# Performance work log

Measured on AMD Instinct MI355X. Metric: run time of the kernel, lower is better.

## Reference

```python
import jax, jax.numpy as jnp
import numpy as np

B, A, F, D, C = 256, 128, 512, 6, 512  # batch, max_atoms, atom_features, max_degree, conv_width


def setup_inputs() -> dict:
    key = jax.random.key(0)
    k1, k2, k3, k4 = jax.random.split(key, 4)
    atoms = jax.random.normal(k1, (B, A, F), dtype=jnp.float32)
    # neighbour indices in [0, A); pad entries beyond each atom's degree with -1
    neigh = jax.random.randint(k2, (B, A, D), 0, A)
    deg = jax.random.randint(k3, (B, A, 1), 0, D)  # degrees in 0..D-1
    bonds = jnp.where(jnp.arange(D)[None, None, :] < deg, neigh, -1)
    # one Dense(conv_width) per degree: stacked kernels [D, F, C] and biases [D, C]
    W = jax.random.normal(k4, (D, F, C), dtype=jnp.float32) * 0.02
    b = jnp.zeros((D, C), dtype=jnp.float32)
    return {"atoms": atoms, "bonds": bonds, "W": W, "b": b}


def reference(atoms, bonds, W, b):
    d_max = bonds.shape[-1]
    # per-atom degree = count of non -1 neighbour slots  [B, A, 1]
    degrees = jnp.sum(bonds != -1, axis=-1, keepdims=True)
    # shift lookup by 1 so that padded (-1) neighbours index a zero row
    padded = jnp.pad(atoms, ((0, 0), (1, 1), (0, 0)))  # [B, A+2, F]
    idx = bonds + 1  # [B, A, D]
    # per-sample gather of neighbour features -> [B, A, D, F]
    neigh_feats = jax.vmap(lambda ref, i: ref[i])(padded, idx)
    summed = jnp.sum(neigh_feats, axis=2) + atoms  # [B, A, F]
    # apply all degree-specific dense layers, then mask-select by degree
    dense = jnp.einsum('baf,dfc->badc', summed, W) + b  # [B, A, D, C]
    masks = (degrees[..., None] == jnp.arange(d_max).reshape(1, 1, d_max, 1)).astype(dense.dtype)
    return jnp.sum(dense * masks, axis=2)  # [B, A, C]
```

## Files before the change

kernel.cpp:

```cpp
#include <hip/hip_runtime.h>
#include <hip/hip_bf16.h>


#define NB 256
#define NA 128
#define NF 512
#define ND 6
#define NC 512
#define NATOMS (NB * NA)

typedef __attribute__((ext_vector_type(8))) short frag8;
typedef __attribute__((ext_vector_type(4))) float f32x4;

static __device__ inline unsigned short f2bu(float f) {
    __hip_bfloat16 h = __float2bfloat16(f);
    return *reinterpret_cast<unsigned short*>(&h);
}
static __device__ inline unsigned int pack2(float a, float b) {
    return (unsigned int)f2bu(a) | ((unsigned int)f2bu(b) << 16);
}
static __device__ inline void async16(const void* g, void* l) {
    __builtin_amdgcn_global_load_lds(
        (const __attribute__((address_space(1))) void*)g,
        (__attribute__((address_space(3))) void*)l, 16, 0, 0);
}

__global__ void transpose_w(const float* __restrict__ W,
                            __hip_bfloat16* __restrict__ Wt) {
    __shared__ float t[32][33];
    const int d  = blockIdx.z;
    const int c0 = blockIdx.x * 32;
    const int f0 = blockIdx.y * 32;
    #pragma unroll
    for (int r = 0; r < 32; r += 8)
        t[threadIdx.y + r][threadIdx.x] =
            W[((size_t)(d * NF + f0 + threadIdx.y + r)) * NC + c0 + threadIdx.x];
    __syncthreads();
    #pragma unroll
    for (int r = 0; r < 32; r += 8)
        Wt[((size_t)(d * NC + c0 + threadIdx.y + r)) * NF + f0 + threadIdx.x] =
            __float2bfloat16(t[threadIdx.x][threadIdx.y + r]);
}

__global__ __launch_bounds__(256) void bucket_atoms(
    const int* __restrict__ bonds, int* __restrict__ counts,
    int* __restrict__ bucket) {
    __shared__ int lcnt[ND];
    __shared__ int lbase[ND];
    const int tid = threadIdx.x;
    if (tid < ND) lcnt[tid] = 0;
    __syncthreads();
    int deg[4], loc[4], gg[4];
    #pragma unroll
    for (int i = 0; i < 4; ++i) {
        int g = blockIdx.x * 1024 + i * 256 + tid;
        gg[i] = g;
        int dg = 0;
        #pragma unroll
        for (int j = 0; j < ND; ++j) dg += (bonds[g * ND + j] >= 0);
        deg[i] = dg;
        loc[i] = atomicAdd(&lcnt[dg], 1);
    }
    __syncthreads();
    if (tid < ND) lbase[tid] = atomicAdd(&counts[tid], lcnt[tid]);
    __syncthreads();
    #pragma unroll
    for (int i = 0; i < 4; ++i)
        bucket[deg[i] * NATOMS + lbase[deg[i]] + loc[i]] = gg[i];
}

__global__ __launch_bounds__(256) void sum_neigh(
    const float* __restrict__ atoms, const int* __restrict__ bonds,
    __hip_bfloat16* __restrict__ summed) {
    const int tid  = threadIdx.x;
    const int wave = tid >> 6;
    const int lane = tid & 63;
    const int g    = blockIdx.x * 4 + wave;
    const float4* a4 = (const float4*)atoms;

    int   nb[ND];
    float msk[ND];
    #pragma unroll
    for (int j = 0; j < ND; ++j) {
        int n = bonds[g * ND + j];
        msk[j] = (n >= 0) ? 1.0f : 0.0f;
        nb[j]  = (n >= 0) ? n : 0;
    }
    const int rowbase = g & ~(NA - 1);

    float4 s0 = a4[(size_t)g * 128 + lane];
    float4 s1 = a4[(size_t)g * 128 + 64 + lane];
    float4 v0[ND], v1[ND];
    #pragma unroll
    for (int j = 0; j < ND; ++j) {
        const size_t base = (size_t)(rowbase + nb[j]) * 128;
        v0[j] = a4[base + lane];
        v1[j] = a4[base + 64 + lane];
    }
    #pragma unroll
    for (int j = 0; j < ND; ++j) {
        s0.x = fmaf(v0[j].x, msk[j], s0.x); s0.y = fmaf(v0[j].y, msk[j], s0.y);
        s0.z = fmaf(v0[j].z, msk[j], s0.z); s0.w = fmaf(v0[j].w, msk[j], s0.w);
        s1.x = fmaf(v1[j].x, msk[j], s1.x); s1.y = fmaf(v1[j].y, msk[j], s1.y);
        s1.z = fmaf(v1[j].z, msk[j], s1.z); s1.w = fmaf(v1[j].w, msk[j], s1.w);
    }

    uint2 o0, o1;
    o0.x = pack2(s0.x, s0.y); o0.y = pack2(s0.z, s0.w);
    o1.x = pack2(s1.x, s1.y); o1.y = pack2(s1.z, s1.w);
    ((uint2*)summed)[(size_t)g * 128 + lane] = o0;
    ((uint2*)summed)[(size_t)g * 128 + 64 + lane] = o1;
}

__global__ __launch_bounds__(256, 4) void gemm_deg(
    const __hip_bfloat16* __restrict__ summed, const __hip_bfloat16* __restrict__ Wt,
    const float* __restrict__ bias, const int* __restrict__ counts,
    const int* __restrict__ bucket, float* __restrict__ out) {
    const int bx = blockIdx.x;
    const int d  = bx % ND;
    const int n0 = (bx / ND) * 128;
    const int Md = counts[d];
    const int m0 = blockIdx.y * 128;
    if (m0 >= Md) return;

    __shared__ __align__(16) __hip_bfloat16 sA[128 * 64];
    __shared__ __align__(16) __hip_bfloat16 sB[128 * 64];
    __shared__ int sRows[128];

    const int tid = threadIdx.x;
    if (tid < 128) {
        int r = m0 + tid;
        sRows[tid] = (r < Md) ? bucket[d * NATOMS + r] : -1;
    }
    __syncthreads();

    const int lane = tid & 63;
    const int w    = tid >> 6;
    const int srow = lane >> 3;
    const int seg  = lane & 7;

    const char* smB = (const char*)summed;
    const char* wtB = (const char*)Wt + (size_t)(d * NC + n0) * (NF * 2);
    size_t gA[4];
    int    rowc[4];
    #pragma unroll
    for (int c = 0; c < 4; ++c) {
        rowc[c] = w * 32 + c * 8 + srow;
        int q = sRows[rowc[c]];
        gA[c] = (size_t)((q < 0) ? 0 : q) * (NF * 2);
    }

    const int quad = lane >> 4, l16 = lane & 15;
    const int wy = w >> 1, wx = w & 1;

    f32x4 acc[4][4];
    #pragma unroll
    for (int i = 0; i < 4; ++i)
        #pragma unroll
        for (int j = 0; j < 4; ++j) acc[i][j] = (f32x4)0.0f;

    for (int kt = 0; kt < NF / 64; ++kt) {
        const int koff = kt * 128 + seg * 16;
        #pragma unroll
        for (int c = 0; c < 4; ++c) {
            async16(smB + gA[c] + koff, &sA[(w * 32 + c * 8) * 64]);
            async16(wtB + (size_t)rowc[c] * (NF * 2) + koff, &sB[(w * 32 + c * 8) * 64]);
        }
        __syncthreads();
        #pragma unroll
        for (int ks = 0; ks < 64; ks += 32) {
            frag8 aF[4], bF[4];
            #pragma unroll
            for (int i = 0; i < 4; ++i)
                aF[i] = *(const frag8*)&sA[(wy * 64 + i * 16 + l16) * 64 + ks + quad * 8];
            #pragma unroll
            for (int j = 0; j < 4; ++j)
                bF[j] = *(const frag8*)&sB[(wx * 64 + j * 16 + l16) * 64 + ks + quad * 8];
            #pragma unroll
            for (int i = 0; i < 4; ++i)
                #pragma unroll
                for (int j = 0; j < 4; ++j)
                    acc[i][j] = __builtin_amdgcn_mfma_f32_16x16x32_bf16(
                        aF[i], bF[j], acc[i][j], 0, 0, 0);
        }
        __syncthreads();
    }

    #pragma unroll
    for (int j = 0; j < 4; ++j) {
        const int n = n0 + wx * 64 + j * 16 + l16;
        const float bv = bias[d * NC + n];
        #pragma unroll
        for (int i = 0; i < 4; ++i) {
            #pragma unroll
            for (int r = 0; r < 4; ++r) {
                const int tr = wy * 64 + i * 16 + quad * 4 + r;
                const int g  = sRows[tr];
                if (g >= 0)
                    out[(size_t)g * NC + n] = acc[i][j][r] + bv;
            }
        }
    }
}

extern "C" void kernel_launch(void* const* d_in, const int* in_sizes, int n_in,
                              void* d_out, int out_size, void* d_ws, size_t ws_size,
                              hipStream_t stream) {
    const float* atoms = (const float*)d_in[0];
    const int*   bonds = (const int*)d_in[1];
    const float* W     = (const float*)d_in[2];
    const float* bias  = (const float*)d_in[3];
    float* out = (float*)d_out;

    char* ws = (char*)d_ws;
    int* counts = (int*)ws;
    int* bucket = (int*)(ws + 1024);
    __hip_bfloat16* Wt     = (__hip_bfloat16*)(ws + 1024 + 786432);
    __hip_bfloat16* summed = (__hip_bfloat16*)(ws + 1024 + 786432 + 3145728);

    hipMemsetAsync(counts, 0, 1024, stream);

    transpose_w<<<dim3(NC / 32, NF / 32, ND), dim3(32, 8), 0, stream>>>(W, Wt);

    bucket_atoms<<<NATOMS / 1024, 256, 0, stream>>>(bonds, counts, bucket);

    sum_neigh<<<NATOMS / 4, 256, 0, stream>>>(atoms, bonds, summed);

    gemm_deg<<<dim3(24, NATOMS / 128), 256, 0, stream>>>(
        summed, Wt, bias, counts, bucket, out);
}
```

Measured before the change: 184.2 us.

## Double-buffer GEMM LDS tiles, swizzle block order, fold counts memset into transpose

The degree-bucketed GEMM now uses two LDS buffers so global-to-LDS async loads for the next K tile are issued before computing the current tile. Launch bounds drop to 2 waves per SIMD to fit the doubled shared memory. The grid index is remapped so consecutive blocks share N tiles and degree groups for better L2 reuse, and sum_neigh blocks are swizzled across the atom range. The separate memset of counts is removed and its zeroing is folded into the transpose kernel to save a launch. Lower occupancy could offset the overlap gains.

```diff
diff --git a/kernel.cpp b/kernel.cpp
--- a/kernel.cpp
+++ b/kernel.cpp
@@ -26,7 +26,11 @@
 }
 
 __global__ void transpose_w(const float* __restrict__ W,
-                            __hip_bfloat16* __restrict__ Wt) {
+                            __hip_bfloat16* __restrict__ Wt,
+                            int* __restrict__ counts) {
+    if (blockIdx.x == 0 && blockIdx.y == 0 && blockIdx.z == 0 &&
+        threadIdx.y == 0 && threadIdx.x < ND)
+        counts[threadIdx.x] = 0;
     __shared__ float t[32][33];
     const int d  = blockIdx.z;
     const int c0 = blockIdx.x * 32;
@@ -75,7 +79,8 @@
     const int tid  = threadIdx.x;
     const int wave = tid >> 6;
     const int lane = tid & 63;
-    const int g    = blockIdx.x * 4 + wave;
+    const int swz  = (blockIdx.x & 7) * (NATOMS / 4 / 8) + (blockIdx.x >> 3);
+    const int g    = swz * 4 + wave;
     const float4* a4 = (const float4*)atoms;
 
     int   nb[ND];
@@ -112,19 +117,21 @@
     ((uint2*)summed)[(size_t)g * 128 + 64 + lane] = o1;
 }
 
-__global__ __launch_bounds__(256, 4) void gemm_deg(
+__global__ __launch_bounds__(256, 2) void gemm_deg(
     const __hip_bfloat16* __restrict__ summed, const __hip_bfloat16* __restrict__ Wt,
     const float* __restrict__ bias, const int* __restrict__ counts,
     const int* __restrict__ bucket, float* __restrict__ out) {
-    const int bx = blockIdx.x;
-    const int d  = bx % ND;
-    const int n0 = (bx / ND) * 128;
+    const int L  = blockIdx.x + 24 * blockIdx.y;
+    const int q  = L >> 3;
+    const int p  = ((q >> 2) << 3) + (L & 7);
+    const int d  = p % ND;
+    const int m0 = (p / ND) * 128;
+    const int n0 = (q & 3) * 128;
     const int Md = counts[d];
-    const int m0 = blockIdx.y * 128;
     if (m0 >= Md) return;
 
-    __shared__ __align__(16) __hip_bfloat16 sA[128 * 64];
-    __shared__ __align__(16) __hip_bfloat16 sB[128 * 64];
+    __shared__ __align__(16) __hip_bfloat16 sA[2][128 * 64];
+    __shared__ __align__(16) __hip_bfloat16 sB[2][128 * 64];
     __shared__ int sRows[128];
 
     const int tid = threadIdx.x;
@@ -146,8 +153,8 @@
     #pragma unroll
     for (int c = 0; c < 4; ++c) {
         rowc[c] = w * 32 + c * 8 + srow;
-        int q = sRows[rowc[c]];
-        gA[c] = (size_t)((q < 0) ? 0 : q) * (NF * 2);
+        int qr = sRows[rowc[c]];
+        gA[c] = (size_t)((qr < 0) ? 0 : qr) * (NF * 2);
     }
 
     const int quad = lane >> 4, l16 = lane & 15;
@@ -159,23 +166,24 @@
         #pragma unroll
         for (int j = 0; j < 4; ++j) acc[i][j] = (f32x4)0.0f;
 
-    for (int kt = 0; kt < NF / 64; ++kt) {
+    auto stage = [&](int buf, int kt) {
         const int koff = kt * 128 + seg * 16;
         #pragma unroll
         for (int c = 0; c < 4; ++c) {
-            async16(smB + gA[c] + koff, &sA[(w * 32 + c * 8) * 64]);
-            async16(wtB + (size_t)rowc[c] * (NF * 2) + koff, &sB[(w * 32 + c * 8) * 64]);
+            async16(smB + gA[c] + koff, &sA[buf][(w * 32 + c * 8) * 64]);
+            async16(wtB + (size_t)rowc[c] * (NF * 2) + koff, &sB[buf][(w * 32 + c * 8) * 64]);
         }
-        __syncthreads();
+    };
+    auto compute = [&](int buf) {
         #pragma unroll
         for (int ks = 0; ks < 64; ks += 32) {
             frag8 aF[4], bF[4];
             #pragma unroll
             for (int i = 0; i < 4; ++i)
-                aF[i] = *(const frag8*)&sA[(wy * 64 + i * 16 + l16) * 64 + ks + quad * 8];
+                aF[i] = *(const frag8*)&sA[buf][(wy * 64 + i * 16 + l16) * 64 + ks + quad * 8];
             #pragma unroll
             for (int j = 0; j < 4; ++j)
-                bF[j] = *(const frag8*)&sB[(wx * 64 + j * 16 + l16) * 64 + ks + quad * 8];
+                bF[j] = *(const frag8*)&sB[buf][(wx * 64 + j * 16 + l16) * 64 + ks + quad * 8];
             #pragma unroll
             for (int i = 0; i < 4; ++i)
                 #pragma unroll
@@ -183,8 +191,19 @@
                     acc[i][j] = __builtin_amdgcn_mfma_f32_16x16x32_bf16(
                         aF[i], bF[j], acc[i][j], 0, 0, 0);
         }
+    };
+
+    stage(0, 0);
+    __syncthreads();
+    int cur = 0;
+    #pragma unroll
+    for (int kt = 1; kt < NF / 64; ++kt) {
+        stage(cur ^ 1, kt);
+        compute(cur);
         __syncthreads();
-    }
+        cur ^= 1;
+    }
+    compute(cur);
 
     #pragma unroll
     for (int j = 0; j < 4; ++j) {
@@ -218,9 +237,7 @@
     __hip_bfloat16* Wt     = (__hip_bfloat16*)(ws + 1024 + 786432);
     __hip_bfloat16* summed = (__hip_bfloat16*)(ws + 1024 + 786432 + 3145728);
 
-    hipMemsetAsync(counts, 0, 1024, stream);
-
-    transpose_w<<<dim3(NC / 32, NF / 32, ND), dim3(32, 8), 0, stream>>>(W, Wt);
+    transpose_w<<<dim3(NC / 32, NF / 32, ND), dim3(32, 8), 0, stream>>>(W, Wt, counts);
 
     bucket_atoms<<<NATOMS / 1024, 256, 0, stream>>>(bonds, counts, bucket);
 
```

Result: slower. 199.1 us (+8.1%).
